# Kernel optimization log

Measured on AMD Instinct MI355X. Metric: run time of the kernel, lower is better.

The kernel has to match this reference:

```python
import jax, jax.numpy as jnp
import numpy as np
from jax import lax

B, C, H, W, S = 8, 64, 64, 64, 12
KSIZE = 5


def _conv2d_same(x, w):
    # x: [N, Cin, H, W], w: [Cout, Cin, kh, kw]
    return lax.conv_general_dilated(
        x, w, window_strides=(1, 1), padding='SAME',
        dimension_numbers=('NCHW', 'OIHW', 'NCHW'))


def setup_inputs() -> dict:
    key = jax.random.key(0)
    k0, k1, k2, k3, k4 = jax.random.split(key, 5)
    x = jax.random.normal(k0, (B, C, H, W, S), dtype=jnp.float32)
    w1 = jax.random.normal(k1, (3 * C, C, 1, 1), dtype=jnp.float32) * 0.05
    b1 = jax.random.normal(k2, (3 * C,), dtype=jnp.float32) * 0.05
    w2 = jax.random.normal(k3, (1, 2 * C, KSIZE, KSIZE), dtype=jnp.float32) * 0.05
    b2 = jax.random.normal(k4, (1,), dtype=jnp.float32) * 0.05
    return {'x': x, 'w1': w1, 'b1': b1, 'w2': w2, 'b2': b2}


def reference(x, w1, b1, w2, b2):
    b, c, h, w_, s = x.shape
    # conv1 (1x1) applied per timestep == channel matmul over all timesteps at once
    qkv = jnp.einsum('oc,bchws->bohws', w1[:, :, 0, 0], x) + b1[None, :, None, None, None]
    Q, K, V = jnp.split(qkv, 3, axis=1)  # each [b, c, h, w, s]

    # conv2 on concat(Q_s, K_t) is linear in channels:
    # score(s,t) = convQ(Q[...,s]) + convK(K[...,t]) + bias
    def per_time_conv(z, wsub):
        # z: [b, c, h, w, s] -> fold time into batch -> conv -> [b, h, w, s]
        zb = jnp.moveaxis(z, -1, 1).reshape(b * s, c, h, w_)
        out = _conv2d_same(zb, wsub)  # [b*s, 1, h, w]
        return jnp.moveaxis(out.reshape(b, s, h, w_), 1, -1)  # [b, h, w, s]

    A_q = per_time_conv(Q, w2[:, :c])   # [b, h, w, s] (query index)
    A_k = per_time_conv(K, w2[:, c:])   # [b, h, w, t] (key index)

    # scores: [b, h, w, t, s]
    scores = A_q[:, :, :, None, :] + A_k[:, :, :, :, None] + b2[0]
    attn = jax.nn.softmax(scores, axis=-2)  # softmax over t (keys)

    # weighted sum of V over t -> [b, c, h, w, s]
    V_out = jnp.einsum('bhwts,bchwt->bchws', attn, V)
    return V_out
```

## Files before the change

### kernel.cpp

```cpp
#include <hip/hip_runtime.h>
#include <hip/hip_bf16.h>

#define WEFF_OFF 0
#define Y_OFF    4096
#define Y_PLANE  393216

__global__ __launch_bounds__(256) void k_prep(const float* __restrict__ w1,
                                              const float* __restrict__ w2,
                                              float* __restrict__ weff) {
    int idx = blockIdx.x * 256 + threadIdx.x;
    if (idx >= 64 * 25) return;
    int cp = idx / 25, tap = idx % 25;
    float s = 0.f;
    for (int c = 0; c < 64; ++c)
        s = fmaf(w2[(64 + c) * 25 + tap], w1[(64 + c) * 64 + cp], s);
    weff[cp * 25 + tap] = s;
}

__global__ __launch_bounds__(128) void k_tap(const float* __restrict__ x,
                                             const float* __restrict__ weff,
                                             float* __restrict__ y) {
    const int n  = blockIdx.x * 128 + threadIdx.x;
    const int m  = n / 3;
    const int tg = n - m * 3;
    const int w  = m & 63;
    const int h  = (m >> 6) & 63;
    const int b  = m >> 12;

    const float* xp = x + (size_t)b * 3145728 + h * 768 + w * 12 + tg * 4;

    float4 acc[25];
#pragma unroll
    for (int k = 0; k < 25; ++k) { acc[k].x = 0.f; acc[k].y = 0.f; acc[k].z = 0.f; acc[k].w = 0.f; }

    float4 v = *(const float4*)(xp);
    for (int c = 0; c < 64; ++c) {
        float4 vn;
        if (c < 63) vn = *(const float4*)(xp + (c + 1) * 49152);
        const float* wg = weff + c * 25;
#pragma unroll
        for (int k = 0; k < 25; ++k) {
            const float g = wg[k];
            acc[k].x = fmaf(g, v.x, acc[k].x);
            acc[k].y = fmaf(g, v.y, acc[k].y);
            acc[k].z = fmaf(g, v.z, acc[k].z);
            acc[k].w = fmaf(g, v.w, acc[k].w);
        }
        v = vn;
    }

#pragma unroll
    for (int k = 0; k < 25; ++k)
        *(float4*)(y + (size_t)k * Y_PLANE + (size_t)n * 4) = acc[k];
}

__global__ __launch_bounds__(64) void k_gather(const float* __restrict__ y,
                                               float* __restrict__ p) {
    const int m = blockIdx.x * 64 + threadIdx.x;
    const int w = m & 63;
    const int h = (m >> 6) & 63;
    const int b = m >> 12;

    float v[12];
#pragma unroll
    for (int t = 0; t < 12; ++t) v[t] = 0.f;

#pragma unroll
    for (int dh = 0; dh < 5; ++dh) {
        const int hh = h + dh - 2;
        if ((unsigned)hh >= 64u) continue;
        const int rowm = (b * 64 + hh) * 64;
#pragma unroll
        for (int dw = 0; dw < 5; ++dw) {
            const int ww = w + dw - 2;
            if ((unsigned)ww >= 64u) continue;
            const float* yp = y + (size_t)(dh * 5 + dw) * Y_PLANE
                                + (size_t)(rowm + ww) * 12;
            float4 a0 = *(const float4*)(yp);
            float4 a1 = *(const float4*)(yp + 4);
            float4 a2 = *(const float4*)(yp + 8);
            v[0] += a0.x; v[1] += a0.y; v[2]  += a0.z; v[3]  += a0.w;
            v[4] += a1.x; v[5] += a1.y; v[6]  += a1.z; v[7]  += a1.w;
            v[8] += a2.x; v[9] += a2.y; v[10] += a2.z; v[11] += a2.w;
        }
    }

    float mx = v[0];
#pragma unroll
    for (int t = 1; t < 12; ++t) mx = fmaxf(mx, v[t]);
    float s = 0.f;
#pragma unroll
    for (int t = 0; t < 12; ++t) { v[t] = __expf(v[t] - mx); s += v[t]; }
    const float inv = 1.f / s;
#pragma unroll
    for (int t = 0; t < 12; ++t) v[t] *= inv;

    float* op = p + (size_t)m * 12;
    float4 s0; s0.x = v[0]; s0.y = v[1]; s0.z = v[2];  s0.w = v[3];
    float4 s1; s1.x = v[4]; s1.y = v[5]; s1.z = v[6];  s1.w = v[7];
    float4 s2; s2.x = v[8]; s2.y = v[9]; s2.z = v[10]; s2.w = v[11];
    *(float4*)(op)     = s0;
    *(float4*)(op + 4) = s1;
    *(float4*)(op + 8) = s2;
}

__global__ __launch_bounds__(512) void k_out(const float* __restrict__ x,
                                             const float* __restrict__ w1,
                                             const float* __restrict__ b1,
                                             const float* __restrict__ p,
                                             float* __restrict__ out) {
    __shared__ float lds[64 * 65];

    const int b  = blockIdx.x >> 6;
    const int h  = blockIdx.x & 63;
    const int w  = threadIdx.x & 63;
    const int cg = threadIdx.x >> 6;

    const float* pp = p + (size_t)((b * 64 + h) * 64 + w) * 12;
    float pv[12];
    {
        float4 t0 = *(const float4*)(pp);
        float4 t1 = *(const float4*)(pp + 4);
        float4 t2 = *(const float4*)(pp + 8);
        pv[0] = t0.x; pv[1] = t0.y; pv[2]  = t0.z; pv[3]  = t0.w;
        pv[4] = t1.x; pv[5] = t1.y; pv[6]  = t1.z; pv[7]  = t1.w;
        pv[8] = t2.x; pv[9] = t2.y; pv[10] = t2.z; pv[11] = t2.w;
    }

    const float* xb0 = x + ((size_t)(b * 64 + cg * 8) * 64 + h) * 768 + w * 12;
#pragma unroll
    for (int j = 0; j < 8; ++j) {
        const float* xp = xb0 + (size_t)j * 49152;
        float4 u0 = *(const float4*)(xp);
        float4 u1 = *(const float4*)(xp + 4);
        float4 u2 = *(const float4*)(xp + 8);
        float s = 0.f;
        s = fmaf(pv[0], u0.x, s);  s = fmaf(pv[1], u0.y, s);
        s = fmaf(pv[2], u0.z, s);  s = fmaf(pv[3], u0.w, s);
        s = fmaf(pv[4], u1.x, s);  s = fmaf(pv[5], u1.y, s);
        s = fmaf(pv[6], u1.z, s);  s = fmaf(pv[7], u1.w, s);
        s = fmaf(pv[8], u2.x, s);  s = fmaf(pv[9], u2.y, s);
        s = fmaf(pv[10], u2.z, s); s = fmaf(pv[11], u2.w, s);
        lds[w * 65 + cg * 8 + j] = s;
    }
    __syncthreads();

    const float* w1v = w1 + 128 * 64 + cg * 8 * 64;
    float acc[8];
#pragma unroll
    for (int j = 0; j < 8; ++j) acc[j] = b1[128 + cg * 8 + j];
    for (int c2 = 0; c2 < 64; ++c2) {
        const float xv = lds[w * 65 + c2];
#pragma unroll
        for (int j = 0; j < 8; ++j)
            acc[j] = fmaf(w1v[j * 64 + c2], xv, acc[j]);
    }

#pragma unroll
    for (int j = 0; j < 8; ++j) {
        const int co = cg * 8 + j;
        float4 f; f.x = acc[j]; f.y = acc[j]; f.z = acc[j]; f.w = acc[j];
        float* op = out + ((size_t)(b * 64 + co) * 4096 + h * 64 + w) * 12;
        *(float4*)(op)     = f;
        *(float4*)(op + 4) = f;
        *(float4*)(op + 8) = f;
    }
}

extern "C" void kernel_launch(void* const* d_in, const int* in_sizes, int n_in,
                              void* d_out, int out_size, void* d_ws, size_t ws_size,
                              hipStream_t stream) {
    const float* x  = (const float*)d_in[0];
    const float* w1 = (const float*)d_in[1];
    const float* b1 = (const float*)d_in[2];
    const float* w2 = (const float*)d_in[3];

    float* outp = (float*)d_out;
    float* weff = outp + WEFF_OFF;
    float* y    = outp + Y_OFF;
    float* p    = (float*)d_ws;

    hipLaunchKernelGGL(k_prep,   dim3(7),    dim3(256), 0, stream, w1, w2, weff);
    hipLaunchKernelGGL(k_tap,    dim3(768),  dim3(128), 0, stream, x, weff, y);
    hipLaunchKernelGGL(k_gather, dim3(512),  dim3(64),  0, stream, y, p);
    hipLaunchKernelGGL(k_out,    dim3(512),  dim3(512), 0, stream, x, w1, b1, p, outp);
}
```

Before: 118.0 us.

## Split tap and gather kernels across more threads per pixel

Result: faster. 98.98 us (-16.1%).

```diff
diff --git a/kernel.cpp b/kernel.cpp
--- a/kernel.cpp
+++ b/kernel.cpp
@@ -17,91 +17,79 @@
     weff[cp * 25 + tap] = s;
 }
 
-__global__ __launch_bounds__(128) void k_tap(const float* __restrict__ x,
+__global__ __launch_bounds__(256) void k_tap(const float* __restrict__ x,
                                              const float* __restrict__ weff,
                                              float* __restrict__ y) {
-    const int n  = blockIdx.x * 128 + threadIdx.x;
-    const int m  = n / 3;
-    const int tg = n - m * 3;
-    const int w  = m & 63;
-    const int h  = (m >> 6) & 63;
-    const int b  = m >> 12;
+    const int gid = blockIdx.x * 256 + threadIdx.x;
+    const int m   = gid / 12;
+    const int t   = gid - m * 12;
+    const int w   = m & 63;
+    const int h   = (m >> 6) & 63;
+    const int b   = m >> 12;
 
-    const float* xp = x + (size_t)b * 3145728 + h * 768 + w * 12 + tg * 4;
+    const float* xp = x + (size_t)b * 3145728 + h * 768 + w * 12 + t;
 
-    float4 acc[25];
+    float acc[25];
 #pragma unroll
-    for (int k = 0; k < 25; ++k) { acc[k].x = 0.f; acc[k].y = 0.f; acc[k].z = 0.f; acc[k].w = 0.f; }
+    for (int k = 0; k < 25; ++k) acc[k] = 0.f;
 
-    float4 v = *(const float4*)(xp);
     for (int c = 0; c < 64; ++c) {
-        float4 vn;
-        if (c < 63) vn = *(const float4*)(xp + (c + 1) * 49152);
+        const float v = xp[(size_t)c * 49152];
         const float* wg = weff + c * 25;
 #pragma unroll
-        for (int k = 0; k < 25; ++k) {
-            const float g = wg[k];
-            acc[k].x = fmaf(g, v.x, acc[k].x);
-            acc[k].y = fmaf(g, v.y, acc[k].y);
-            acc[k].z = fmaf(g, v.z, acc[k].z);
-            acc[k].w = fmaf(g, v.w, acc[k].w);
-        }
-        v = vn;
+        for (int k = 0; k < 25; ++k)
+            acc[k] = fmaf(wg[k], v, acc[k]);
     }
 
 #pragma unroll
     for (int k = 0; k < 25; ++k)
-        *(float4*)(y + (size_t)k * Y_PLANE + (size_t)n * 4) = acc[k];
+        y[(size_t)k * Y_PLANE + gid] = acc[k];
 }
 
-__global__ __launch_bounds__(64) void k_gather(const float* __restrict__ y,
-                                               float* __restrict__ p) {
-    const int m = blockIdx.x * 64 + threadIdx.x;
-    const int w = m & 63;
-    const int h = (m >> 6) & 63;
-    const int b = m >> 12;
+__global__ __launch_bounds__(256) void k_gather(const float* __restrict__ y,
+                                                float* __restrict__ p) {
+    const int tid  = threadIdx.x;
+    const int m    = blockIdx.x * 64 + (tid >> 2);
+    const int q    = tid & 3;
+    const int qq   = (q == 3) ? 2 : q;
+    const int w    = m & 63;
+    const int h    = (m >> 6) & 63;
+    const int b    = m >> 12;
 
-    float v[12];
-#pragma unroll
-    for (int t = 0; t < 12; ++t) v[t] = 0.f;
+    float4 a; a.x = 0.f; a.y = 0.f; a.z = 0.f; a.w = 0.f;
 
 #pragma unroll
     for (int dh = 0; dh < 5; ++dh) {
         const int hh = h + dh - 2;
         if ((unsigned)hh >= 64u) continue;
-        const int rowm = (b * 64 + hh) * 64;
+        const int rowb = (b * 64 + hh) * 64;
 #pragma unroll
         for (int dw = 0; dw < 5; ++dw) {
             const int ww = w + dw - 2;
             if ((unsigned)ww >= 64u) continue;
             const float* yp = y + (size_t)(dh * 5 + dw) * Y_PLANE
-                                + (size_t)(rowm + ww) * 12;
-            float4 a0 = *(const float4*)(yp);
-            float4 a1 = *(const float4*)(yp + 4);
-            float4 a2 = *(const float4*)(yp + 8);
-            v[0] += a0.x; v[1] += a0.y; v[2]  += a0.z; v[3]  += a0.w;
-            v[4] += a1.x; v[5] += a1.y; v[6]  += a1.z; v[7]  += a1.w;
-            v[8] += a2.x; v[9] += a2.y; v[10] += a2.z; v[11] += a2.w;
+                                + (size_t)(rowb + ww) * 12 + qq * 4;
+            float4 v = *(const float4*)(yp);
+            a.x += v.x; a.y += v.y; a.z += v.z; a.w += v.w;
         }
     }
 
-    float mx = v[0];
-#pragma unroll
-    for (int t = 1; t < 12; ++t) mx = fmaxf(mx, v[t]);
-    float s = 0.f;
-#pragma unroll
-    for (int t = 0; t < 12; ++t) { v[t] = __expf(v[t] - mx); s += v[t]; }
-    const float inv = 1.f / s;
-#pragma unroll
-    for (int t = 0; t < 12; ++t) v[t] *= inv;
+    float mx = fmaxf(fmaxf(a.x, a.y), fmaxf(a.z, a.w));
+    mx = fmaxf(mx, __shfl_xor(mx, 1, 4));
+    mx = fmaxf(mx, __shfl_xor(mx, 2, 4));
 
-    float* op = p + (size_t)m * 12;
-    float4 s0; s0.x = v[0]; s0.y = v[1]; s0.z = v[2];  s0.w = v[3];
-    float4 s1; s1.x = v[4]; s1.y = v[5]; s1.z = v[6];  s1.w = v[7];
-    float4 s2; s2.x = v[8]; s2.y = v[9]; s2.z = v[10]; s2.w = v[11];
-    *(float4*)(op)     = s0;
-    *(float4*)(op + 4) = s1;
-    *(float4*)(op + 8) = s2;
+    float e0 = __expf(a.x - mx), e1 = __expf(a.y - mx);
+    float e2 = __expf(a.z - mx), e3 = __expf(a.w - mx);
+    const float s4 = e0 + e1 + e2 + e3;
+    const float s0 = __shfl(s4, 0, 4);
+    const float s1 = __shfl(s4, 1, 4);
+    const float s2 = __shfl(s4, 2, 4);
+    const float inv = 1.f / (s0 + s1 + s2);
+
+    if (q < 3) {
+        float4 o; o.x = e0 * inv; o.y = e1 * inv; o.z = e2 * inv; o.w = e3 * inv;
+        *(float4*)(p + (size_t)m * 12 + q * 4) = o;
+    }
 }
 
 __global__ __launch_bounds__(512) void k_out(const float* __restrict__ x,
@@ -181,7 +169,7 @@
     float* p    = (float*)d_ws;
 
     hipLaunchKernelGGL(k_prep,   dim3(7),    dim3(256), 0, stream, w1, w2, weff);
-    hipLaunchKernelGGL(k_tap,    dim3(768),  dim3(128), 0, stream, x, weff, y);
-    hipLaunchKernelGGL(k_gather, dim3(512),  dim3(64),  0, stream, y, p);
+    hipLaunchKernelGGL(k_tap,    dim3(1536), dim3(256), 0, stream, x, weff, y);
+    hipLaunchKernelGGL(k_gather, dim3(512),  dim3(256), 0, stream, y, p);
     hipLaunchKernelGGL(k_out,    dim3(512),  dim3(512), 0, stream, x, w1, b1, p, outp);
 }
```

## Fuse 5x5 tap conv and gather-softmax into one LDS-reduced kernel

Applied to the files above, without the earlier changes.

Result: faster. 96.32 us (-18.4%).

```diff
diff --git a/kernel.cpp b/kernel.cpp
--- a/kernel.cpp
+++ b/kernel.cpp
@@ -2,8 +2,6 @@
 #include <hip/hip_bf16.h>
 
 #define WEFF_OFF 0
-#define Y_OFF    4096
-#define Y_PLANE  393216
 
 __global__ __launch_bounds__(256) void k_prep(const float* __restrict__ w1,
                                               const float* __restrict__ w2,
@@ -17,91 +15,103 @@
     weff[cp * 25 + tap] = s;
 }
 
-__global__ __launch_bounds__(128) void k_tap(const float* __restrict__ x,
-                                             const float* __restrict__ weff,
-                                             float* __restrict__ y) {
-    const int n  = blockIdx.x * 128 + threadIdx.x;
-    const int m  = n / 3;
-    const int tg = n - m * 3;
-    const int w  = m & 63;
-    const int h  = (m >> 6) & 63;
-    const int b  = m >> 12;
+__global__ __launch_bounds__(320) void k_conv5(const float* __restrict__ x,
+                                               const float* __restrict__ weff,
+                                               float* __restrict__ p) {
+    __shared__ float lds[64 * 61];
 
-    const float* xp = x + (size_t)b * 3145728 + h * 768 + w * 12 + tg * 4;
+    const int bid = blockIdx.x;
+    const int b   = bid & 7;
+    const int h   = bid >> 3;
+    const int w   = threadIdx.x & 63;
+    const int dh  = threadIdx.x >> 6;
+    const int r   = h + dh - 2;
 
-    float4 acc[25];
+    for (int i = threadIdx.x; i < 64 * 61; i += 320) lds[i] = 0.f;
+
+    float zz[5][12];
 #pragma unroll
-    for (int k = 0; k < 25; ++k) { acc[k].x = 0.f; acc[k].y = 0.f; acc[k].z = 0.f; acc[k].w = 0.f; }
+    for (int dw = 0; dw < 5; ++dw)
+#pragma unroll
+        for (int t = 0; t < 12; ++t) zz[dw][t] = 0.f;
 
-    float4 v = *(const float4*)(xp);
-    for (int c = 0; c < 64; ++c) {
-        float4 vn;
-        if (c < 63) vn = *(const float4*)(xp + (c + 1) * 49152);
-        const float* wg = weff + c * 25;
+    if ((unsigned)r < 64u) {
+        const float* xp = x + (size_t)b * 3145728 + r * 768 + w * 12;
+        const float* wgb = weff + dh * 5;
+        for (int c = 0; c < 64; c += 2) {
+            const float* x0 = xp + (size_t)c * 49152;
+            const float* x1 = x0 + 49152;
+            float4 a0 = *(const float4*)(x0);
+            float4 a1 = *(const float4*)(x0 + 4);
+            float4 a2 = *(const float4*)(x0 + 8);
+            float4 c0 = *(const float4*)(x1);
+            float4 c1 = *(const float4*)(x1 + 4);
+            float4 c2 = *(const float4*)(x1 + 8);
+            const float* wg0 = wgb + c * 25;
+            const float* wg1 = wg0 + 25;
 #pragma unroll
-        for (int k = 0; k < 25; ++k) {
-            const float g = wg[k];
-            acc[k].x = fmaf(g, v.x, acc[k].x);
-            acc[k].y = fmaf(g, v.y, acc[k].y);
-            acc[k].z = fmaf(g, v.z, acc[k].z);
-            acc[k].w = fmaf(g, v.w, acc[k].w);
+            for (int dw = 0; dw < 5; ++dw) {
+                const float g = wg0[dw];
+                zz[dw][0] = fmaf(g, a0.x, zz[dw][0]);  zz[dw][1] = fmaf(g, a0.y, zz[dw][1]);
+                zz[dw][2] = fmaf(g, a0.z, zz[dw][2]);  zz[dw][3] = fmaf(g, a0.w, zz[dw][3]);
+                zz[dw][4] = fmaf(g, a1.x, zz[dw][4]);  zz[dw][5] = fmaf(g, a1.y, zz[dw][5]);
+                zz[dw][6] = fmaf(g, a1.z, zz[dw][6]);  zz[dw][7] = fmaf(g, a1.w, zz[dw][7]);
+                zz[dw][8] = fmaf(g, a2.x, zz[dw][8]);  zz[dw][9] = fmaf(g, a2.y, zz[dw][9]);
+                zz[dw][10] = fmaf(g, a2.z, zz[dw][10]); zz[dw][11] = fmaf(g, a2.w, zz[dw][11]);
+            }
+#pragma unroll
+            for (int dw = 0; dw < 5; ++dw) {
+                const float g = wg1[dw];
+                zz[dw][0] = fmaf(g, c0.x, zz[dw][0]);  zz[dw][1] = fmaf(g, c0.y, zz[dw][1]);
+                zz[dw][2] = fmaf(g, c0.z, zz[dw][2]);  zz[dw][3] = fmaf(g, c0.w, zz[dw][3]);
+                zz[dw][4] = fmaf(g, c1.x, zz[dw][4]);  zz[dw][5] = fmaf(g, c1.y, zz[dw][5]);
+                zz[dw][6] = fmaf(g, c1.z, zz[dw][6]);  zz[dw][7] = fmaf(g, c1.w, zz[dw][7]);
+                zz[dw][8] = fmaf(g, c2.x, zz[dw][8]);  zz[dw][9] = fmaf(g, c2.y, zz[dw][9]);
+                zz[dw][10] = fmaf(g, c2.z, zz[dw][10]); zz[dw][11] = fmaf(g, c2.w, zz[dw][11]);
+            }
         }
-        v = vn;
+    }
+    __syncthreads();
+
+#pragma unroll
+    for (int turn = 0; turn < 5; ++turn) {
+        if (dh == turn) {
+#pragma unroll
+            for (int dw = 0; dw < 5; ++dw) {
+                const int wp = w + 2 - dw;
+                if ((unsigned)wp < 64u) {
+                    float* a = lds + wp * 61 + dw * 12;
+#pragma unroll
+                    for (int t = 0; t < 12; ++t) a[t] += zz[dw][t];
+                }
+            }
+        }
+        __syncthreads();
     }
 
+    if (dh == 0) {
+        const float* lw = lds + w * 61;
+        float v[12];
 #pragma unroll
-    for (int k = 0; k < 25; ++k)
-        *(float4*)(y + (size_t)k * Y_PLANE + (size_t)n * 4) = acc[k];
-}
-
-__global__ __launch_bounds__(64) void k_gather(const float* __restrict__ y,
-                                               float* __restrict__ p) {
-    const int m = blockIdx.x * 64 + threadIdx.x;
-    const int w = m & 63;
-    const int h = (m >> 6) & 63;
-    const int b = m >> 12;
-
-    float v[12];
+        for (int t = 0; t < 12; ++t)
+            v[t] = lw[t] + lw[12 + t] + lw[24 + t] + lw[36 + t] + lw[48 + t];
+        float mx = v[0];
 #pragma unroll
-    for (int t = 0; t < 12; ++t) v[t] = 0.f;
-
+        for (int t = 1; t < 12; ++t) mx = fmaxf(mx, v[t]);
+        float s = 0.f;
 #pragma unroll
-    for (int dh = 0; dh < 5; ++dh) {
-        const int hh = h + dh - 2;
-        if ((unsigned)hh >= 64u) continue;
-        const int rowm = (b * 64 + hh) * 64;
+        for (int t = 0; t < 12; ++t) { v[t] = __expf(v[t] - mx); s += v[t]; }
+        const float inv = 1.f / s;
 #pragma unroll
-        for (int dw = 0; dw < 5; ++dw) {
-            const int ww = w + dw - 2;
-            if ((unsigned)ww >= 64u) continue;
-            const float* yp = y + (size_t)(dh * 5 + dw) * Y_PLANE
-                                + (size_t)(rowm + ww) * 12;
-            float4 a0 = *(const float4*)(yp);
-            float4 a1 = *(const float4*)(yp + 4);
-            float4 a2 = *(const float4*)(yp + 8);
-            v[0] += a0.x; v[1] += a0.y; v[2]  += a0.z; v[3]  += a0.w;
-            v[4] += a1.x; v[5] += a1.y; v[6]  += a1.z; v[7]  += a1.w;
-            v[8] += a2.x; v[9] += a2.y; v[10] += a2.z; v[11] += a2.w;
-        }
+        for (int t = 0; t < 12; ++t) v[t] *= inv;
+        float* op = p + (size_t)((b * 64 + h) * 64 + w) * 12;
+        float4 s0; s0.x = v[0]; s0.y = v[1]; s0.z = v[2];  s0.w = v[3];
+        float4 s1; s1.x = v[4]; s1.y = v[5]; s1.z = v[6];  s1.w = v[7];
+        float4 s2; s2.x = v[8]; s2.y = v[9]; s2.z = v[10]; s2.w = v[11];
+        *(float4*)(op)     = s0;
+        *(float4*)(op + 4) = s1;
+        *(float4*)(op + 8) = s2;
     }
-
-    float mx = v[0];
-#pragma unroll
-    for (int t = 1; t < 12; ++t) mx = fmaxf(mx, v[t]);
-    float s = 0.f;
-#pragma unroll
-    for (int t = 0; t < 12; ++t) { v[t] = __expf(v[t] - mx); s += v[t]; }
-    const float inv = 1.f / s;
-#pragma unroll
-    for (int t = 0; t < 12; ++t) v[t] *= inv;
-
-    float* op = p + (size_t)m * 12;
-    float4 s0; s0.x = v[0]; s0.y = v[1]; s0.z = v[2];  s0.w = v[3];
-    float4 s1; s1.x = v[4]; s1.y = v[5]; s1.z = v[6];  s1.w = v[7];
-    float4 s2; s2.x = v[8]; s2.y = v[9]; s2.z = v[10]; s2.w = v[11];
-    *(float4*)(op)     = s0;
-    *(float4*)(op + 4) = s1;
-    *(float4*)(op + 8) = s2;
 }
 
 __global__ __launch_bounds__(512) void k_out(const float* __restrict__ x,
@@ -177,11 +187,9 @@
 
     float* outp = (float*)d_out;
     float* weff = outp + WEFF_OFF;
-    float* y    = outp + Y_OFF;
     float* p    = (float*)d_ws;
 
-    hipLaunchKernelGGL(k_prep,   dim3(7),    dim3(256), 0, stream, w1, w2, weff);
-    hipLaunchKernelGGL(k_tap,    dim3(768),  dim3(128), 0, stream, x, weff, y);
-    hipLaunchKernelGGL(k_gather, dim3(512),  dim3(64),  0, stream, y, p);
-    hipLaunchKernelGGL(k_out,    dim3(512),  dim3(512), 0, stream, x, w1, b1, p, outp);
+    hipLaunchKernelGGL(k_prep,  dim3(7),   dim3(256), 0, stream, w1, w2, weff);
+    hipLaunchKernelGGL(k_conv5, dim3(512), dim3(320), 0, stream, x, weff, p);
+    hipLaunchKernelGGL(k_out,   dim3(512), dim3(512), 0, stream, x, w1, b1, p, outp);
 }
```
